# Kernel optimization log

Hardware: AMD Instinct MI355X
Metric: run time of the kernel (lower is better)

The kernel has to match this reference:

```python
import jax, jax.numpy as jnp
import numpy as np

N_NODES = 50000
N_EDGES = 800000
NODE_DIM = 128
EDGE_DIM = 10
IN_DIM = 2 * NODE_DIM + EDGE_DIM
BN_EPS = 1e-5


def setup_inputs() -> dict:
    key = jax.random.key(0)
    ks = jax.random.split(key, 8)
    h = jax.random.normal(ks[0], (N_NODES, NODE_DIM), dtype=jnp.float32)
    edge_index = jax.random.randint(ks[1], (2, N_EDGES), 0, N_NODES, dtype=jnp.int64)
    edge_feat = jax.random.normal(ks[2], (N_EDGES, EDGE_DIM), dtype=jnp.float32)
    scale = 1.0 / np.sqrt(IN_DIM)
    gate_w = jax.random.normal(ks[3], (IN_DIM, NODE_DIM), dtype=jnp.float32) * scale
    gate_b = jax.random.normal(ks[4], (NODE_DIM,), dtype=jnp.float32) * scale
    cand_w = jax.random.normal(ks[5], (IN_DIM, NODE_DIM), dtype=jnp.float32) * scale
    cand_b = jax.random.normal(ks[6], (NODE_DIM,), dtype=jnp.float32) * scale
    bn_gamma = jnp.ones((NODE_DIM,), dtype=jnp.float32)
    bn_beta = jnp.zeros((NODE_DIM,), dtype=jnp.float32)
    return {"h": h, "edge_index": edge_index, "edge_feat": edge_feat,
            "gate_w": gate_w, "gate_b": gate_b, "cand_w": cand_w, "cand_b": cand_b,
            "bn_gamma": bn_gamma, "bn_beta": bn_beta}


def reference(h, edge_index, edge_feat, gate_w, gate_b, cand_w, cand_b, bn_gamma, bn_beta):
    src = edge_index[0]
    dst = edge_index[1]
    # gather endpoint features and concat with edge features: [E, 2*D + De]
    z = jnp.concatenate([h[src], h[dst], edge_feat], axis=1)
    g = jax.nn.sigmoid(z @ gate_w + gate_b)   # [E, D]
    c = jax.nn.softplus(z @ cand_w + cand_b)  # [E, D]
    m = g * c
    # scatter-add messages to source nodes (matches index_add_(0, src, m))
    agg = jax.ops.segment_sum(m, src, num_segments=h.shape[0])
    # BatchNorm1d in training mode: batch mean / biased variance over nodes
    mean = jnp.mean(agg, axis=0)
    var = jnp.var(agg, axis=0)
    agg_bn = (agg - mean) * jax.lax.rsqrt(var + BN_EPS) * bn_gamma + bn_beta
    return jax.nn.softplus(h + agg_bn)
```

## Files before the change

### kernel.cpp

```cpp
#include <hip/hip_runtime.h>
#include <math.h>

#define N_NODES 50000
#define N_EDGES 800000
#define D 128
#define DE 10
#define TE 64
#define N_TILES (N_EDGES / TE)
#define SST 132
#define ASTR 136
#define OST 520
#define WP2_ELEMS (4 * 32 * 64 * 8)
#define WEF_ELEMS (16 * 64 * 8)
#define SCAN_BLOCKS 196
#define CSTRIDE 16
#define SCAT_BLOCKS 1563
#define GEMM_BLOCKS 782

typedef __bf16 bf16x8 __attribute__((ext_vector_type(8)));
typedef __bf16 bf16x4 __attribute__((ext_vector_type(4)));
typedef __bf16 bf16x2 __attribute__((ext_vector_type(2)));
typedef float  f32x4  __attribute__((ext_vector_type(4)));

__device__ __forceinline__ float fast_sigmoid(float x) {
    float t = __builtin_amdgcn_exp2f(-1.44269504089f * x);
    return __builtin_amdgcn_rcpf(1.0f + t);
}
__device__ __forceinline__ float fast_softplus(float x) {
    float t = __builtin_amdgcn_exp2f(-1.44269504089f * fabsf(x));
    return fmaxf(x, 0.0f) + 0.69314718056f * __builtin_amdgcn_logf(1.0f + t);
}
__device__ __forceinline__ float bflo(unsigned int u) {
    return __builtin_bit_cast(float, u << 16);
}
__device__ __forceinline__ float bfhi(unsigned int u) {
    return __builtin_bit_cast(float, u & 0xFFFF0000u);
}

__global__ __launch_bounds__(256) void prep(
    const float* __restrict__ gw, const float* __restrict__ cw,
    const int* __restrict__ ei,
    __bf16* __restrict__ wp2, __bf16* __restrict__ wef,
    int* __restrict__ counts, unsigned short* __restrict__ rank)
{
    int bx = blockIdx.x, t = threadIdx.x;
    if (bx < 256) {
        int idx = bx * 256 + t;
        int j    = idx & 7;
        int lane = (idx >> 3) & 63;
        int nb   = (idx >> 9) & 31;
        int kb   = idx >> 14;
        int k    = kb * 32 + ((lane >> 4) << 3) + j;
        int jp   = nb * 16 + (lane & 15);
        float v;
        if      (jp < 128) v = gw[k * D + jp];
        else if (jp < 256) v = cw[k * D + (jp - 128)];
        else if (jp < 384) v = gw[(128 + k) * D + (jp - 256)];
        else               v = cw[(128 + k) * D + (jp - 384)];
        wp2[idx] = (__bf16)v;
    } else if (bx < 288) {
        int idx = (bx - 256) * 256 + t;
        int j    = idx & 7;
        int lane = (idx >> 3) & 63;
        int nb   = idx >> 9;
        int k    = ((lane >> 4) << 3) + j;
        int col  = (nb >> 1) * 16 + (lane & 15);
        const float* w = (nb & 1) ? cw : gw;
        wef[idx] = (__bf16)((k < 10) ? w[(256 + k) * D + col] : 0.0f);
    } else {
        int e = (bx - 288) * 256 + t;
        int r = atomicAdd(&counts[ei[e] * CSTRIDE], 1);
        rank[e] = (unsigned short)r;
    }
}

__global__ __launch_bounds__(256) void scan_partials(
    const int* __restrict__ counts, int* __restrict__ bsum)
{
    __shared__ int ss[256];
    int t = threadIdx.x;
    int i = blockIdx.x * 256 + t;
    int c = (i < N_NODES) ? counts[i * CSTRIDE] : 0;
    ss[t] = c;
    __syncthreads();
    #pragma unroll
    for (int off = 1; off < 256; off <<= 1) {
        int v = (t >= off) ? ss[t - off] : 0;
        __syncthreads();
        ss[t] += v;
        __syncthreads();
    }
    if (t == 255) bsum[blockIdx.x] = ss[255];
}

__global__ __launch_bounds__(256) void scan_final(
    const int* __restrict__ counts, const int* __restrict__ bsum,
    int* __restrict__ excl)
{
    __shared__ int sb[256];
    __shared__ int ss[256];
    int t = threadIdx.x;
    sb[t] = (t < SCAN_BLOCKS) ? bsum[t] : 0;
    int i = blockIdx.x * 256 + t;
    int c = (i < N_NODES) ? counts[i * CSTRIDE] : 0;
    ss[t] = c;
    __syncthreads();
    #pragma unroll
    for (int off = 1; off < 256; off <<= 1) {
        int v  = (t >= off) ? ss[t - off] : 0;
        int vb = (t >= off) ? sb[t - off] : 0;
        __syncthreads();
        ss[t] += v;
        sb[t] += vb;
        __syncthreads();
    }
    int base = blockIdx.x ? sb[blockIdx.x - 1] : 0;
    if (i < N_NODES) excl[i] = base + ss[t] - c;
}

__global__ __launch_bounds__(512, 4) void scatter_gemm(
    const int* __restrict__ ei, const unsigned short* __restrict__ rank,
    const int* __restrict__ excl, int* __restrict__ perm,
    const float* __restrict__ h, const __bf16* __restrict__ wp2,
    unsigned int* __restrict__ paI, unsigned int* __restrict__ pbI)
{
    if (blockIdx.x < SCAT_BLOCKS) {
        int e = blockIdx.x * 512 + threadIdx.x;
        if (e < N_EDGES) {
            int node = ei[e];
            perm[excl[node] + (int)rank[e]] = e;
        }
        return;
    }

    __shared__ __align__(16) __bf16 sm[64 * OST];
    __bf16* za = sm;
    const int t  = threadIdx.x;
    const int r0 = (blockIdx.x - SCAT_BLOCKS) * 64;

    #pragma unroll
    for (int it = 0; it < 4; ++it) {
        int ch  = it * 512 + t;
        int row = ch >> 5, cs = ch & 31;
        int node = r0 + row;
        float4 v = (node < N_NODES) ? *(const float4*)&h[(size_t)node * D + cs * 4]
                                    : make_float4(0.f, 0.f, 0.f, 0.f);
        bf16x4 o = { (__bf16)v.x, (__bf16)v.y, (__bf16)v.z, (__bf16)v.w };
        *(bf16x4*)&za[row * ASTR + cs * 4] = o;
    }
    __syncthreads();

    const int w = t >> 6, l = t & 63, quad = l >> 4, col16 = l & 15;
    f32x4 acc[4][4];
    #pragma unroll
    for (int mt = 0; mt < 4; ++mt)
        #pragma unroll
        for (int nt = 0; nt < 4; ++nt)
            acc[mt][nt] = (f32x4)0.0f;

    const __bf16* zp = &za[col16 * ASTR + quad * 8];
    const __bf16* bp = &wp2[(size_t)((w * 4) * 64 + l) * 8];

    #pragma unroll
    for (int kb = 0; kb < 4; ++kb) {
        bf16x8 afr[4];
        #pragma unroll
        for (int mt = 0; mt < 4; ++mt)
            afr[mt] = *(const bf16x8*)&zp[mt * 16 * ASTR + kb * 32];
        bf16x8 bfr[4];
        #pragma unroll
        for (int nt = 0; nt < 4; ++nt)
            bfr[nt] = *(const bf16x8*)&bp[(size_t)(kb * 32 + nt) * 512];
        #pragma unroll
        for (int mt = 0; mt < 4; ++mt)
            #pragma unroll
            for (int nt = 0; nt < 4; ++nt)
                acc[mt][nt] = __builtin_amdgcn_mfma_f32_16x16x32_bf16(
                    afr[mt], bfr[nt], acc[mt][nt], 0, 0, 0);
    }
    __syncthreads();

    #pragma unroll
    for (int mt = 0; mt < 4; ++mt)
        #pragma unroll
        for (int nt = 0; nt < 4; ++nt)
            #pragma unroll
            for (int r = 0; r < 4; ++r) {
                int row  = mt * 16 + quad * 4 + r;
                int colj = (w * 4 + nt) * 16 + col16;
                sm[row * OST + colj] = (__bf16)acc[mt][nt][r];
            }
    __syncthreads();

    #pragma unroll
    for (int it = 0; it < 8; ++it) {
        int ch   = it * 512 + t;
        int row  = ch >> 6;
        int sub  = ch & 63;
        int hp   = sub >> 5;
        int c0   = (sub & 31) * 4;
        int node = r0 + row;
        if (node < N_NODES) {
            const __bf16* sr = &sm[row * OST + hp * 256];
            bf16x4 gl = *(const bf16x4*)&sr[c0];
            bf16x4 cl = *(const bf16x4*)&sr[128 + c0];
            unsigned int wds[4];
            #pragma unroll
            for (int i = 0; i < 4; ++i) {
                bf16x2 pr = { gl[i], cl[i] };
                wds[i] = __builtin_bit_cast(unsigned int, pr);
            }
            unsigned int* dp = hp ? pbI : paI;
            *(uint4*)&dp[(size_t)node * 128 + c0] = *(const uint4*)&wds[0];
        }
    }
}

__global__ __launch_bounds__(512, 6) void edge_fuse(
    const unsigned int* __restrict__ paI, const unsigned int* __restrict__ pbI,
    const int* __restrict__ perm, const int* __restrict__ ei,
    const float* __restrict__ ef, const __bf16* __restrict__ wef,
    const float* __restrict__ gb, const float* __restrict__ cb,
    float* __restrict__ agg)
{
    __shared__ __align__(16) float ms[TE * SST];
    __shared__ __align__(16) __bf16 zE[TE * 32];
    __shared__ int s_src[TE], s_dst[TE];

    const int t  = threadIdx.x;
    const int e0 = blockIdx.x * TE;
    const int w = t >> 6, l = t & 63, quad = l >> 4, col16 = l & 15;

    const __bf16* wpp = &wef[(size_t)((w * 2) * 64 + l) * 8];
    bf16x8 bfr0 = *(const bf16x8*)&wpp[0];
    bf16x8 bfr1 = *(const bf16x8*)&wpp[512];
    const int c = w * 16 + col16;
    const float gbv = gb[c], cbv = cb[c];

    if (t < TE) {
        int p = perm[e0 + t];
        s_src[t] = ei[p];
        s_dst[t] = ei[N_EDGES + p];
        const float* efr = &ef[(size_t)p * DE];
        __bf16* row = &zE[t * 32];
        #pragma unroll
        for (int j = 0; j < 5; ++j) {
            float2 a = *(const float2*)&efr[j * 2];
            bf16x2 pr = { (__bf16)a.x, (__bf16)a.y };
            *(bf16x2*)&row[j * 2] = pr;
        }
        *(bf16x2*)&row[10] = (bf16x2)(__bf16)0.0f;
        *(bf16x4*)&row[12] = (bf16x4)(__bf16)0.0f;
        *(bf16x8*)&row[16] = (bf16x8)(__bf16)0.0f;
        *(bf16x8*)&row[24] = (bf16x8)(__bf16)0.0f;
    }
    __syncthreads();

    f32x4 acc[4][2];
    #pragma unroll
    for (int mt = 0; mt < 4; ++mt) {
        const bf16x8 a = *(const bf16x8*)&zE[(mt * 16 + col16) * 32 + quad * 8];
        acc[mt][0] = __builtin_amdgcn_mfma_f32_16x16x32_bf16(a, bfr0, (f32x4)0.0f, 0, 0, 0);
        acc[mt][1] = __builtin_amdgcn_mfma_f32_16x16x32_bf16(a, bfr1, (f32x4)0.0f, 0, 0, 0);
    }

    #pragma unroll
    for (int mt = 0; mt < 4; ++mt) {
        unsigned int uA[4], uB[4];
        #pragma unroll
        for (int r = 0; r < 4; ++r) {
            int e = mt * 16 + quad * 4 + r;
            uA[r] = paI[(size_t)s_src[e] * 128 + c];
            uB[r] = pbI[(size_t)s_dst[e] * 128 + c];
        }
        #pragma unroll
        for (int r = 0; r < 4; ++r) {
            int e = mt * 16 + quad * 4 + r;
            float g = bflo(uA[r]) + bflo(uB[r]) + acc[mt][0][r] + gbv;
            float x = bfhi(uA[r]) + bfhi(uB[r]) + acc[mt][1][r] + cbv;
            ms[e * SST + c] = fast_sigmoid(g) * fast_softplus(x);
        }
    }
    __syncthreads();

    const int seg = t >> 7;
    const int cc  = t & 127;
    const int rlo = seg * 16, rhi = rlo + 16;
    int   cur = s_src[rlo];
    float s   = 0.0f;
    for (int e = rlo; e < rhi; ++e) {
        int node = s_src[e];
        float v  = ms[e * SST + cc];
        if (node != cur) {
            atomicAdd(&agg[(size_t)cur * D + cc], s);
            s = 0.0f; cur = node;
        }
        s += v;
    }
    atomicAdd(&agg[(size_t)cur * D + cc], s);
}

__global__ __launch_bounds__(256) void col_stats(
    const float* __restrict__ agg, float* __restrict__ stats)
{
    const int t    = threadIdx.x;
    const int col  = t & 127;
    const int half = t >> 7;
    float s = 0.0f, s2 = 0.0f;
    for (int r = blockIdx.x * 2 + half; r < N_NODES; r += gridDim.x * 2) {
        float v = agg[(size_t)r * D + col];
        s += v; s2 += v * v;
    }
    atomicAdd(&stats[col], s);
    atomicAdd(&stats[128 + col], s2);
}

__global__ __launch_bounds__(256) void out_softplus(
    const float* __restrict__ h, const float* __restrict__ agg,
    const float* __restrict__ stats, const float* __restrict__ gamma,
    const float* __restrict__ beta, float* __restrict__ out)
{
    __shared__ float sc[128], bi[128];
    int t = threadIdx.x;
    if (t < 128) {
        const float inv_n = 1.0f / (float)N_NODES;
        float mean = stats[t] * inv_n;
        float var  = stats[128 + t] * inv_n - mean * mean;
        var = fmaxf(var, 0.0f);
        float rstd = rsqrtf(var + 1e-5f);
        float s = rstd * gamma[t];
        sc[t] = s;
        bi[t] = beta[t] - mean * s;
    }
    __syncthreads();
    int idx4 = blockIdx.x * 256 + t;
    int base = idx4 * 4;
    if (base < N_NODES * D) {
        float4 hv = *(const float4*)&h[base];
        float4 av = *(const float4*)&agg[base];
        int c = base & 127;
        float4 o;
        o.x = fast_softplus(hv.x + av.x * sc[c + 0] + bi[c + 0]);
        o.y = fast_softplus(hv.y + av.y * sc[c + 1] + bi[c + 1]);
        o.z = fast_softplus(hv.z + av.z * sc[c + 2] + bi[c + 2]);
        o.w = fast_softplus(hv.w + av.w * sc[c + 3] + bi[c + 3]);
        *(float4*)&out[base] = o;
    }
}

extern "C" void kernel_launch(void* const* d_in, const int* in_sizes, int n_in,
                              void* d_out, int out_size, void* d_ws, size_t ws_size,
                              hipStream_t stream) {
    const float* h     = (const float*)d_in[0];
    const int*   ei    = (const int*)  d_in[1];
    const float* ef    = (const float*)d_in[2];
    const float* gw    = (const float*)d_in[3];
    const float* gb    = (const float*)d_in[4];
    const float* cw    = (const float*)d_in[5];
    const float* cb    = (const float*)d_in[6];
    const float* gamma = (const float*)d_in[7];
    const float* beta  = (const float*)d_in[8];
    float* out = (float*)d_out;

    float*          agg    = (float*)d_ws;
    float*          stats  = agg + (size_t)N_NODES * D;
    int*            counts = (int*)(stats + 256);
    unsigned int*   pbI    = (unsigned int*)counts;
    char*           afterU = (char*)counts + (size_t)N_NODES * 128 * sizeof(unsigned int);
    __bf16*         wp2    = (__bf16*)afterU;
    __bf16*         wef    = wp2 + WP2_ELEMS;
    int*            bsum   = (int*)(wef + WEF_ELEMS);
    int*            excl   = bsum + 256;
    unsigned short* rank   = (unsigned short*)(excl + N_NODES);
    int*            perm   = (int*)(rank + N_EDGES);
    unsigned int*   paI    = (unsigned int*)d_out;

    const size_t zero_bytes = ((size_t)N_NODES * D + 256) * sizeof(float)
                            + (size_t)N_NODES * CSTRIDE * sizeof(int);
    hipMemsetAsync(d_ws, 0, zero_bytes, stream);
    prep<<<3413, 256, 0, stream>>>(gw, cw, ei, wp2, wef, counts, rank);
    scan_partials<<<SCAN_BLOCKS, 256, 0, stream>>>(counts, bsum);
    scan_final<<<SCAN_BLOCKS, 256, 0, stream>>>(counts, bsum, excl);
    scatter_gemm<<<SCAT_BLOCKS + GEMM_BLOCKS, 512, 0, stream>>>(
        ei, rank, excl, perm, h, wp2, paI, pbI);
    edge_fuse<<<N_TILES, 512, 0, stream>>>(paI, pbI, perm, ei, ef, wef, gb, cb, agg);
    col_stats<<<784, 256, 0, stream>>>(agg, stats);
    out_softplus<<<N_NODES * D / 4 / 256, 256, 0, stream>>>(
        h, agg, stats, gamma, beta, out);
}
```

Before: 346.5 us.

## Pack src/dst/edge ids in atomic-cursor sort and fold agg zeroing into prep

After: 381.2 us. 1.1x slower.

```diff
diff --git a/kernel.cpp b/kernel.cpp
--- a/kernel.cpp
+++ b/kernel.cpp
@@ -14,6 +14,7 @@
 #define WEF_ELEMS (16 * 64 * 8)
 #define SCAN_BLOCKS 196
 #define CSTRIDE 16
+#define CURST 2
 #define SCAT_BLOCKS 1563
 #define GEMM_BLOCKS 782
 
@@ -41,7 +42,7 @@
     const float* __restrict__ gw, const float* __restrict__ cw,
     const int* __restrict__ ei,
     __bf16* __restrict__ wp2, __bf16* __restrict__ wef,
-    int* __restrict__ counts, unsigned short* __restrict__ rank)
+    int* __restrict__ counts, float4* __restrict__ aggz)
 {
     int bx = blockIdx.x, t = threadIdx.x;
     if (bx < 256) {
@@ -67,10 +68,12 @@
         int col  = (nb >> 1) * 16 + (lane & 15);
         const float* w = (nb & 1) ? cw : gw;
         wef[idx] = (__bf16)((k < 10) ? w[(256 + k) * D + col] : 0.0f);
+    } else if (bx < 3413) {
+        int e = (bx - 288) * 256 + t;
+        atomicAdd(&counts[ei[e] * CSTRIDE], 1);
     } else {
-        int e = (bx - 288) * 256 + t;
-        int r = atomicAdd(&counts[ei[e] * CSTRIDE], 1);
-        rank[e] = (unsigned short)r;
+        int i = (bx - 3413) * 256 + t;
+        aggz[i] = make_float4(0.f, 0.f, 0.f, 0.f);
     }
 }
 
@@ -95,7 +98,7 @@
 
 __global__ __launch_bounds__(256) void scan_final(
     const int* __restrict__ counts, const int* __restrict__ bsum,
-    int* __restrict__ excl)
+    int* __restrict__ cursor)
 {
     __shared__ int sb[256];
     __shared__ int ss[256];
@@ -115,12 +118,12 @@
         __syncthreads();
     }
     int base = blockIdx.x ? sb[blockIdx.x - 1] : 0;
-    if (i < N_NODES) excl[i] = base + ss[t] - c;
+    if (i < N_NODES) cursor[i * CURST] = base + ss[t] - c;
 }
 
 __global__ __launch_bounds__(512, 4) void scatter_gemm(
-    const int* __restrict__ ei, const unsigned short* __restrict__ rank,
-    const int* __restrict__ excl, int* __restrict__ perm,
+    const int* __restrict__ ei, int* __restrict__ cursor,
+    int2* __restrict__ sde,
     const float* __restrict__ h, const __bf16* __restrict__ wp2,
     unsigned int* __restrict__ paI, unsigned int* __restrict__ pbI)
 {
@@ -128,7 +131,8 @@
         int e = blockIdx.x * 512 + threadIdx.x;
         if (e < N_EDGES) {
             int node = ei[e];
-            perm[excl[node] + (int)rank[e]] = e;
+            int pos = atomicAdd(&cursor[node * CURST], 1);
+            sde[pos] = make_int2(node | (ei[N_EDGES + e] << 16), e);
         }
         return;
     }
@@ -218,8 +222,8 @@
 
 __global__ __launch_bounds__(512, 6) void edge_fuse(
     const unsigned int* __restrict__ paI, const unsigned int* __restrict__ pbI,
-    const int* __restrict__ perm, const int* __restrict__ ei,
-    const float* __restrict__ ef, const __bf16* __restrict__ wef,
+    const int2* __restrict__ sde, const float* __restrict__ ef,
+    const __bf16* __restrict__ wef,
     const float* __restrict__ gb, const float* __restrict__ cb,
     float* __restrict__ agg)
 {
@@ -238,10 +242,10 @@
     const float gbv = gb[c], cbv = cb[c];
 
     if (t < TE) {
-        int p = perm[e0 + t];
-        s_src[t] = ei[p];
-        s_dst[t] = ei[N_EDGES + p];
-        const float* efr = &ef[(size_t)p * DE];
+        int2 p = sde[e0 + t];
+        s_src[t] = p.x & 0xFFFF;
+        s_dst[t] = (p.x >> 16) & 0xFFFF;
+        const float* efr = &ef[(size_t)p.y * DE];
         __bf16* row = &zE[t * 32];
         #pragma unroll
         for (int j = 0; j < 5; ++j) {
@@ -362,28 +366,27 @@
     const float* beta  = (const float*)d_in[8];
     float* out = (float*)d_out;
 
-    float*          agg    = (float*)d_ws;
-    float*          stats  = agg + (size_t)N_NODES * D;
-    int*            counts = (int*)(stats + 256);
-    unsigned int*   pbI    = (unsigned int*)counts;
-    char*           afterU = (char*)counts + (size_t)N_NODES * 128 * sizeof(unsigned int);
-    __bf16*         wp2    = (__bf16*)afterU;
-    __bf16*         wef    = wp2 + WP2_ELEMS;
-    int*            bsum   = (int*)(wef + WEF_ELEMS);
-    int*            excl   = bsum + 256;
-    unsigned short* rank   = (unsigned short*)(excl + N_NODES);
-    int*            perm   = (int*)(rank + N_EDGES);
-    unsigned int*   paI    = (unsigned int*)d_out;
-
-    const size_t zero_bytes = ((size_t)N_NODES * D + 256) * sizeof(float)
-                            + (size_t)N_NODES * CSTRIDE * sizeof(int);
-    hipMemsetAsync(d_ws, 0, zero_bytes, stream);
-    prep<<<3413, 256, 0, stream>>>(gw, cw, ei, wp2, wef, counts, rank);
+    float*        agg    = (float*)d_ws;
+    float*        stats  = agg + (size_t)N_NODES * D;
+    int*          counts = (int*)(stats + 256);
+    unsigned int* pbI    = (unsigned int*)counts;
+    char*         afterU = (char*)counts + (size_t)N_NODES * 128 * sizeof(unsigned int);
+    __bf16*       wp2    = (__bf16*)afterU;
+    __bf16*       wef    = wp2 + WP2_ELEMS;
+    int*          bsum   = (int*)(wef + WEF_ELEMS);
+    int*          cursor = bsum + 256;
+    int2*         sde    = (int2*)(cursor + N_NODES * CURST);
+    unsigned int* paI    = (unsigned int*)d_out;
+
+    hipMemsetAsync(stats, 0,
+                   256 * sizeof(float) + (size_t)N_NODES * CSTRIDE * sizeof(int),
+                   stream);
+    prep<<<9663, 256, 0, stream>>>(gw, cw, ei, wp2, wef, counts, (float4*)agg);
     scan_partials<<<SCAN_BLOCKS, 256, 0, stream>>>(counts, bsum);
-    scan_final<<<SCAN_BLOCKS, 256, 0, stream>>>(counts, bsum, excl);
+    scan_final<<<SCAN_BLOCKS, 256, 0, stream>>>(counts, bsum, cursor);
     scatter_gemm<<<SCAT_BLOCKS + GEMM_BLOCKS, 512, 0, stream>>>(
-        ei, rank, excl, perm, h, wp2, paI, pbI);
-    edge_fuse<<<N_TILES, 512, 0, stream>>>(paI, pbI, perm, ei, ef, wef, gb, cb, agg);
+        ei, cursor, sde, h, wp2, paI, pbI);
+    edge_fuse<<<N_TILES, 512, 0, stream>>>(paI, pbI, sde, ef, wef, gb, cb, agg);
     col_stats<<<784, 256, 0, stream>>>(agg, stats);
     out_softplus<<<N_NODES * D / 4 / 256, 256, 0, stream>>>(
         h, agg, stats, gamma, beta, out);
```

## Compress edge index arrays and vectorize endpoint gather in edge kernel

Applied to the files above, without the earlier changes.

Measured after the change: 568.3 us. 64.0% more time.

```diff
diff --git a/kernel.cpp b/kernel.cpp
--- a/kernel.cpp
+++ b/kernel.cpp
@@ -21,6 +21,7 @@
 typedef __bf16 bf16x4 __attribute__((ext_vector_type(4)));
 typedef __bf16 bf16x2 __attribute__((ext_vector_type(2)));
 typedef float  f32x4  __attribute__((ext_vector_type(4)));
+typedef unsigned int u32x4 __attribute__((ext_vector_type(4)));
 
 __device__ __forceinline__ float fast_sigmoid(float x) {
     float t = __builtin_amdgcn_exp2f(-1.44269504089f * x);
@@ -41,7 +42,7 @@
     const float* __restrict__ gw, const float* __restrict__ cw,
     const int* __restrict__ ei,
     __bf16* __restrict__ wp2, __bf16* __restrict__ wef,
-    int* __restrict__ counts, unsigned short* __restrict__ rank)
+    int* __restrict__ counts, unsigned char* __restrict__ rank)
 {
     int bx = blockIdx.x, t = threadIdx.x;
     if (bx < 256) {
@@ -70,7 +71,7 @@
     } else {
         int e = (bx - 288) * 256 + t;
         int r = atomicAdd(&counts[ei[e] * CSTRIDE], 1);
-        rank[e] = (unsigned short)r;
+        rank[e] = (unsigned char)r;
     }
 }
 
@@ -95,7 +96,7 @@
 
 __global__ __launch_bounds__(256) void scan_final(
     const int* __restrict__ counts, const int* __restrict__ bsum,
-    int* __restrict__ excl)
+    int* __restrict__ anchors, unsigned short* __restrict__ excl16)
 {
     __shared__ int sb[256];
     __shared__ int ss[256];
@@ -114,13 +115,15 @@
         sb[t] += vb;
         __syncthreads();
     }
-    int base = blockIdx.x ? sb[blockIdx.x - 1] : 0;
-    if (i < N_NODES) excl[i] = base + ss[t] - c;
+    if (t == 0) anchors[blockIdx.x] = blockIdx.x ? sb[blockIdx.x - 1] : 0;
+    if (i < N_NODES) excl16[i] = (unsigned short)(ss[t] - c);
 }
 
 __global__ __launch_bounds__(512, 4) void scatter_gemm(
-    const int* __restrict__ ei, const unsigned short* __restrict__ rank,
-    const int* __restrict__ excl, int* __restrict__ perm,
+    const int* __restrict__ ei, const unsigned char* __restrict__ rank,
+    const int* __restrict__ anchors, const unsigned short* __restrict__ excl16,
+    unsigned int* __restrict__ sdx, unsigned short* __restrict__ eidlo,
+    unsigned char* __restrict__ eidhi,
     const float* __restrict__ h, const __bf16* __restrict__ wp2,
     unsigned int* __restrict__ paI, unsigned int* __restrict__ pbI)
 {
@@ -128,7 +131,10 @@
         int e = blockIdx.x * 512 + threadIdx.x;
         if (e < N_EDGES) {
             int node = ei[e];
-            perm[excl[node] + (int)rank[e]] = e;
+            int pos = anchors[node >> 8] + (int)excl16[node] + (int)rank[e];
+            sdx[pos]   = (unsigned int)node | ((unsigned int)ei[N_EDGES + e] << 16);
+            eidlo[pos] = (unsigned short)e;
+            eidhi[pos] = (unsigned char)(e >> 16);
         }
         return;
     }
@@ -218,12 +224,13 @@
 
 __global__ __launch_bounds__(512, 6) void edge_fuse(
     const unsigned int* __restrict__ paI, const unsigned int* __restrict__ pbI,
-    const int* __restrict__ perm, const int* __restrict__ ei,
+    const unsigned int* __restrict__ sdx, const unsigned short* __restrict__ eidlo,
+    const unsigned char* __restrict__ eidhi,
     const float* __restrict__ ef, const __bf16* __restrict__ wef,
     const float* __restrict__ gb, const float* __restrict__ cb,
     float* __restrict__ agg)
 {
-    __shared__ __align__(16) float ms[TE * SST];
+    __shared__ __align__(16) unsigned int sbuf[TE * SST];
     __shared__ __align__(16) __bf16 zE[TE * 32];
     __shared__ int s_src[TE], s_dst[TE];
 
@@ -238,10 +245,11 @@
     const float gbv = gb[c], cbv = cb[c];
 
     if (t < TE) {
-        int p = perm[e0 + t];
-        s_src[t] = ei[p];
-        s_dst[t] = ei[N_EDGES + p];
-        const float* efr = &ef[(size_t)p * DE];
+        unsigned int sd = sdx[e0 + t];
+        int eid = (int)eidlo[e0 + t] | ((int)eidhi[e0 + t] << 16);
+        s_src[t] = (int)(sd & 0xFFFFu);
+        s_dst[t] = (int)(sd >> 16);
+        const float* efr = &ef[(size_t)eid * DE];
         __bf16* row = &zE[t * 32];
         #pragma unroll
         for (int j = 0; j < 5; ++j) {
@@ -256,48 +264,64 @@
     }
     __syncthreads();
 
-    f32x4 acc[4][2];
+    #pragma unroll
+    for (int it = 0; it < 2; ++it) {
+        int id  = it * 512 + t;
+        int e   = id >> 4, grp = id & 15;
+        int src = s_src[e], dst = s_dst[e];
+        int c0  = grp * 8;
+        u32x4 a0 = *(const u32x4*)&paI[(size_t)src * 128 + c0];
+        u32x4 a1 = *(const u32x4*)&paI[(size_t)src * 128 + c0 + 4];
+        u32x4 b0 = *(const u32x4*)&pbI[(size_t)dst * 128 + c0];
+        u32x4 b1 = *(const u32x4*)&pbI[(size_t)dst * 128 + c0 + 4];
+        unsigned int o[8];
+        #pragma unroll
+        for (int j = 0; j < 4; ++j) {
+            bf16x2 p0 = { (__bf16)(bflo(a0[j]) + bflo(b0[j])),
+                          (__bf16)(bfhi(a0[j]) + bfhi(b0[j])) };
+            bf16x2 p1 = { (__bf16)(bflo(a1[j]) + bflo(b1[j])),
+                          (__bf16)(bfhi(a1[j]) + bfhi(b1[j])) };
+            o[j]     = __builtin_bit_cast(unsigned int, p0);
+            o[j + 4] = __builtin_bit_cast(unsigned int, p1);
+        }
+        *(uint4*)&sbuf[e * SST + c0]     = *(const uint4*)&o[0];
+        *(uint4*)&sbuf[e * SST + c0 + 4] = *(const uint4*)&o[4];
+    }
+    __syncthreads();
+
+    const f32x4 bg4 = { gbv, gbv, gbv, gbv };
+    const f32x4 bc4 = { cbv, cbv, cbv, cbv };
+    f32x4 accg[4], accc[4];
     #pragma unroll
     for (int mt = 0; mt < 4; ++mt) {
         const bf16x8 a = *(const bf16x8*)&zE[(mt * 16 + col16) * 32 + quad * 8];
-        acc[mt][0] = __builtin_amdgcn_mfma_f32_16x16x32_bf16(a, bfr0, (f32x4)0.0f, 0, 0, 0);
-        acc[mt][1] = __builtin_amdgcn_mfma_f32_16x16x32_bf16(a, bfr1, (f32x4)0.0f, 0, 0, 0);
+        accg[mt] = __builtin_amdgcn_mfma_f32_16x16x32_bf16(a, bfr0, bg4, 0, 0, 0);
+        accc[mt] = __builtin_amdgcn_mfma_f32_16x16x32_bf16(a, bfr1, bc4, 0, 0, 0);
     }
 
     #pragma unroll
     for (int mt = 0; mt < 4; ++mt) {
-        unsigned int uA[4], uB[4];
+        const int eb = mt * 16 + quad * 4;
+        float m[4]; int nd[4];
         #pragma unroll
         for (int r = 0; r < 4; ++r) {
-            int e = mt * 16 + quad * 4 + r;
-            uA[r] = paI[(size_t)s_src[e] * 128 + c];
-            uB[r] = pbI[(size_t)s_dst[e] * 128 + c];
-        }
-        #pragma unroll
-        for (int r = 0; r < 4; ++r) {
-            int e = mt * 16 + quad * 4 + r;
-            float g = bflo(uA[r]) + bflo(uB[r]) + acc[mt][0][r] + gbv;
-            float x = bfhi(uA[r]) + bfhi(uB[r]) + acc[mt][1][r] + cbv;
-            ms[e * SST + c] = fast_sigmoid(g) * fast_softplus(x);
-        }
-    }
-    __syncthreads();
-
-    const int seg = t >> 7;
-    const int cc  = t & 127;
-    const int rlo = seg * 16, rhi = rlo + 16;
-    int   cur = s_src[rlo];
-    float s   = 0.0f;
-    for (int e = rlo; e < rhi; ++e) {
-        int node = s_src[e];
-        float v  = ms[e * SST + cc];
-        if (node != cur) {
-            atomicAdd(&agg[(size_t)cur * D + cc], s);
-            s = 0.0f; cur = node;
-        }
-        s += v;
-    }
-    atomicAdd(&agg[(size_t)cur * D + cc], s);
+            unsigned int u = sbuf[(eb + r) * SST + c];
+            float g = bflo(u) + accg[mt][r];
+            float x = bfhi(u) + accc[mt][r];
+            m[r]  = fast_sigmoid(g) * fast_softplus(x);
+            nd[r] = s_src[eb + r];
+        }
+        float s = m[0];
+        #pragma unroll
+        for (int r = 1; r < 4; ++r) {
+            if (nd[r] != nd[r - 1]) {
+                atomicAdd(&agg[(size_t)nd[r - 1] * D + c], s);
+                s = 0.0f;
+            }
+            s += m[r];
+        }
+        atomicAdd(&agg[(size_t)nd[3] * D + c], s);
+    }
 }
 
 __global__ __launch_bounds__(256) void col_stats(
@@ -362,28 +386,32 @@
     const float* beta  = (const float*)d_in[8];
     float* out = (float*)d_out;
 
-    float*          agg    = (float*)d_ws;
-    float*          stats  = agg + (size_t)N_NODES * D;
-    int*            counts = (int*)(stats + 256);
-    unsigned int*   pbI    = (unsigned int*)counts;
-    char*           afterU = (char*)counts + (size_t)N_NODES * 128 * sizeof(unsigned int);
-    __bf16*         wp2    = (__bf16*)afterU;
-    __bf16*         wef    = wp2 + WP2_ELEMS;
-    int*            bsum   = (int*)(wef + WEF_ELEMS);
-    int*            excl   = bsum + 256;
-    unsigned short* rank   = (unsigned short*)(excl + N_NODES);
-    int*            perm   = (int*)(rank + N_EDGES);
-    unsigned int*   paI    = (unsigned int*)d_out;
+    float*          agg     = (float*)d_ws;
+    float*          stats   = agg + (size_t)N_NODES * D;
+    int*            counts  = (int*)(stats + 256);
+    unsigned int*   pbI     = (unsigned int*)counts;
+    char*           afterU  = (char*)counts + (size_t)N_NODES * 128 * sizeof(unsigned int);
+    __bf16*         wp2     = (__bf16*)afterU;
+    __bf16*         wef     = wp2 + WP2_ELEMS;
+    int*            bsum    = (int*)(wef + WEF_ELEMS);
+    int*            anchors = bsum + 256;
+    unsigned short* excl16  = (unsigned short*)(anchors + 256);
+    unsigned char*  rank    = (unsigned char*)(excl16 + N_NODES);
+    unsigned int*   sdx     = (unsigned int*)(rank + N_EDGES);
+    unsigned short* eidlo   = (unsigned short*)(sdx + N_EDGES);
+    unsigned char*  eidhi   = (unsigned char*)(eidlo + N_EDGES);
+    unsigned int*   paI     = (unsigned int*)d_out;
 
     const size_t zero_bytes = ((size_t)N_NODES * D + 256) * sizeof(float)
                             + (size_t)N_NODES * CSTRIDE * sizeof(int);
     hipMemsetAsync(d_ws, 0, zero_bytes, stream);
     prep<<<3413, 256, 0, stream>>>(gw, cw, ei, wp2, wef, counts, rank);
     scan_partials<<<SCAN_BLOCKS, 256, 0, stream>>>(counts, bsum);
-    scan_final<<<SCAN_BLOCKS, 256, 0, stream>>>(counts, bsum, excl);
+    scan_final<<<SCAN_BLOCKS, 256, 0, stream>>>(counts, bsum, anchors, excl16);
     scatter_gemm<<<SCAT_BLOCKS + GEMM_BLOCKS, 512, 0, stream>>>(
-        ei, rank, excl, perm, h, wp2, paI, pbI);
-    edge_fuse<<<N_TILES, 512, 0, stream>>>(paI, pbI, perm, ei, ef, wef, gb, cb, agg);
+        ei, rank, anchors, excl16, sdx, eidlo, eidhi, h, wp2, paI, pbI);
+    edge_fuse<<<N_TILES, 512, 0, stream>>>(
+        paI, pbI, sdx, eidlo, eidhi, ef, wef, gb, cb, agg);
     col_stats<<<784, 256, 0, stream>>>(agg, stats);
     out_softplus<<<N_NODES * D / 4 / 256, 256, 0, stream>>>(
         h, agg, stats, gamma, beta, out);
```
